# Performance work log

Measured on AMD Instinct MI355X. Metric: run time of the kernel, lower is better.

## Reference

```python
import jax, jax.numpy as jnp
import numpy as np

B, S, D, H = 8, 1024, 1024, 16
DH = D // H  # 64
LN_EPS = 1e-5


def setup_inputs() -> dict:
    key = jax.random.key(0)
    ks = jax.random.split(key, 12)
    w = lambda k, shape: (jax.random.normal(k, shape, dtype=jnp.float32) * 0.02)
    return {
        "key": jax.random.normal(ks[0], (B, S, D), dtype=jnp.float32),
        "value": jax.random.normal(ks[1], (B, S, D), dtype=jnp.float32),
        "query": jax.random.normal(ks[2], (B, S, D), dtype=jnp.float32),
        "atten_mask": jax.random.randint(ks[3], (B, S, S), 0, 2).astype(bool),
        "Wk": w(ks[4], (D, D)), "bk": jnp.zeros((D,), jnp.float32),
        "Wv": w(ks[5], (D, D)), "bv": jnp.zeros((D,), jnp.float32),
        "Wq": w(ks[6], (D, D)), "bq": jnp.zeros((D,), jnp.float32),
        "Wf": w(ks[7], (D, D)), "bf": jnp.zeros((D,), jnp.float32),
        "gamma": jnp.ones((D,), jnp.float32),
        "beta": jnp.zeros((D,), jnp.float32),
    }


def reference(key, value, query, atten_mask, Wk, bk, Wv, bv, Wq, bq, Wf, bf, gamma, beta):
    residual = query
    k = key @ Wk + bk      # [B,S,D]
    v = value @ Wv + bv
    q = query @ Wq + bq
    # Faithful to the original: raw .view(B*H, -1, d) reshape, NO head transpose.
    k = k.reshape(B * H, S, DH)
    v = v.reshape(B * H, S, DH)
    q = q.reshape(B * H, S, DH)
    # torch .repeat(H,1,1) tiles along batch dim -> head bh uses mask[bh % B]
    mask = jnp.tile(atten_mask, (H, 1, 1))  # [B*H, S, S]
    scale = (DH // H) ** (-0.5)  # quirky original scaling: (64//16)**-0.5 = 0.5
    scores = jnp.einsum('bqd,bkd->bqk', q, k) * scale  # [B*H, S, S]
    scores = jnp.where(mask, jnp.float32(-1e6), scores)
    attention = jax.nn.softmax(scores, axis=2)
    context = jnp.einsum('bqk,bkd->bqd', attention, v)  # [B*H, S, DH]
    context = context.reshape(B, S, D)
    out = context @ Wf + bf
    out = residual + out
    # LayerNorm over last dim
    mu = jnp.mean(out, axis=-1, keepdims=True)
    var = jnp.var(out, axis=-1, keepdims=True)
    out = (out - mu) * jax.lax.rsqrt(var + LN_EPS) * gamma + beta
    return out, attention
```

## Files before the change

### kernel.cpp

```cpp
#include <hip/hip_runtime.h>


typedef unsigned short u16;
typedef unsigned long long u64;
typedef __attribute__((ext_vector_type(8))) short bf16x8;
typedef __attribute__((ext_vector_type(4))) float f32x4;

#define MFMA_BF16(a, b, c) __builtin_amdgcn_mfma_f32_16x16x32_bf16((a), (b), (c), 0, 0, 0)

__device__ __forceinline__ u16 f2bf(float f) {
  unsigned u = __float_as_uint(f);
  u += 0x7fffu + ((u >> 16) & 1u);
  return (u16)(u >> 16);
}
__device__ __forceinline__ float bf2f(u16 b) {
  return __uint_as_float(((unsigned)b) << 16);
}
__device__ __forceinline__ unsigned cvt_pk_bf16(float lo, float hi) {
  unsigned r;
  asm("v_cvt_pk_bf16_f32 %0, %1, %2" : "=v"(r) : "v"(lo), "v"(hi));
  return r;
}
__device__ __forceinline__ void gload_lds16(const u16* g, u16* l) {
  __builtin_amdgcn_global_load_lds(
      (const __attribute__((address_space(1))) void*)g,
      (__attribute__((address_space(3))) void*)l, 16, 0, 0);
}

static constexpr size_t MD = 8192ull * 1024ull;
static constexpr size_t DD = 1024ull * 1024ull;
static constexpr float SCL = 0.72134752044f;

__global__ __launch_bounds__(256) void cvt_k(const float* __restrict__ K,
                                             const float* __restrict__ V,
                                             const float* __restrict__ Q,
                                             u16* __restrict__ O) {
  const int z = blockIdx.z;
  const float* src = (z == 0) ? K : ((z == 1) ? V : Q);
  const size_t i = ((size_t)blockIdx.x * 256 + threadIdx.x) * 4;
  const float4 v = *reinterpret_cast<const float4*>(src + i);
  ushort4 o;
  o.x = f2bf(v.x); o.y = f2bf(v.y); o.z = f2bf(v.z); o.w = f2bf(v.w);
  *reinterpret_cast<ushort4*>(O + (size_t)z * MD + i) = o;
}

__global__ __launch_bounds__(256) void wt_k(const float* __restrict__ Wk,
                                            const float* __restrict__ Wv,
                                            const float* __restrict__ Wq,
                                            const float* __restrict__ Wf,
                                            u16* __restrict__ WT) {
  const int z = blockIdx.z;
  const float* W = (z == 0) ? Wk : ((z == 1) ? Wv : ((z == 2) ? Wq : Wf));
  __shared__ float tile[32][33];
  const int k0 = blockIdx.y * 32, n0 = blockIdx.x * 32;
  const int r = threadIdx.x >> 5, c = threadIdx.x & 31;
#pragma unroll
  for (int rr = r; rr < 32; rr += 8)
    tile[rr][c] = W[(size_t)(k0 + rr) * 1024 + n0 + c];
  __syncthreads();
#pragma unroll
  for (int rr = r; rr < 32; rr += 8)
    WT[(size_t)z * DD + (size_t)(n0 + rr) * 1024 + k0 + c] = f2bf(tile[c][rr]);
}

__global__ __launch_bounds__(256) void mb_k(const unsigned char* __restrict__ mask8,
                                            u64* __restrict__ mb) {
  __shared__ int mflag;
  if (threadIdx.x == 0) {
    const unsigned* mw = reinterpret_cast<const unsigned*>(mask8);
    int allW = 1;
    for (int i = 0; i < 64; ++i) {
      const unsigned v = mw[i];
      if (v != 0u && v != 1u && v != 0x3F800000u) allW = 0;
    }
    mflag = allW;
  }
  __syncthreads();
  const int wide = mflag;
  const size_t wi = (size_t)blockIdx.x * 256 + threadIdx.x;
  const size_t src0 = wi * 64;
  u64 bits = 0ull;
  if (!wide) {
    const uint4* p = reinterpret_cast<const uint4*>(mask8 + src0);
#pragma unroll
    for (int q = 0; q < 4; ++q) {
      const uint4 v = p[q];
      const unsigned vv[4] = {v.x, v.y, v.z, v.w};
#pragma unroll
      for (int k = 0; k < 4; ++k) {
        unsigned tt = vv[k];
        tt |= tt >> 4; tt |= tt >> 2; tt |= tt >> 1;
        tt &= 0x01010101u;
        const unsigned nib =
            (tt & 1u) | ((tt >> 7) & 2u) | ((tt >> 14) & 4u) | ((tt >> 21) & 8u);
        bits |= (u64)nib << (q * 16 + k * 4);
      }
    }
  } else {
    const unsigned* p = reinterpret_cast<const unsigned*>(mask8) + src0;
#pragma unroll
    for (int k = 0; k < 64; ++k)
      bits |= (u64)(p[k] != 0u) << k;
  }
  mb[wi] = bits;
}

template <int EPI>
__global__ __launch_bounds__(256) void gemm_bt(
    const u16* __restrict__ A0, const u16* __restrict__ B0,
    const float* __restrict__ bias0, const float* __restrict__ bias1,
    const float* __restrict__ bias2, u16* __restrict__ Obf,
    const float* __restrict__ resid) {
  __shared__ __align__(16) u16 As[128 * 32];
  __shared__ __align__(16) u16 Bs[128 * 32];
  const int z = blockIdx.z;
  const u16* A = A0 + (size_t)z * MD;
  const u16* Bt = B0 + (size_t)z * DD;
  const float* bias = (z == 0) ? bias0 : ((z == 1) ? bias1 : bias2);
  const int t = threadIdx.x;
  const int m0 = blockIdx.y * 128, n0 = blockIdx.x * 128;
  const int w = t >> 6, lane = t & 63, lr = lane & 15, lk = lane >> 4;
  const int wm = (w >> 1) * 64, wn = (w & 1) * 64;
  const int srow = lane >> 2, scol = (lane & 3) * 8;

  f32x4 acc[4][4] = {};

  for (int k0 = 0; k0 < 1024; k0 += 32) {
    __syncthreads();
#pragma unroll
    for (int it = 0; it < 2; ++it) {
      const int c = w * 2 + it;
      gload_lds16(A + (size_t)(m0 + 16 * c + srow) * 1024 + k0 + scol,
                  &As[c * 512 + lane * 8]);
      gload_lds16(Bt + (size_t)(n0 + 16 * c + srow) * 1024 + k0 + scol,
                  &Bs[c * 512 + lane * 8]);
    }
    __syncthreads();
    bf16x8 af[4], bfr[4];
#pragma unroll
    for (int i = 0; i < 4; ++i)
      af[i] = *reinterpret_cast<const bf16x8*>(&As[(wm + i * 16 + lr) * 32 + lk * 8]);
#pragma unroll
    for (int j = 0; j < 4; ++j)
      bfr[j] = *reinterpret_cast<const bf16x8*>(&Bs[(wn + j * 16 + lr) * 32 + lk * 8]);
#pragma unroll
    for (int i = 0; i < 4; ++i) {
#pragma unroll
      for (int j = 0; j < 4; ++j)
        acc[i][j] = MFMA_BF16(af[i], bfr[j], acc[i][j]);
    }
  }

#pragma unroll
  for (int i = 0; i < 4; ++i) {
#pragma unroll
    for (int j = 0; j < 4; ++j) {
#pragma unroll
      for (int r = 0; r < 4; ++r) {
        const int row = m0 + wm + i * 16 + lk * 4 + r;
        const int col = n0 + wn + j * 16 + lr;
        const size_t idx = (size_t)row * 1024 + col;
        const float v = acc[i][j][r] + bias[col];
        if constexpr (EPI == 0) {
          Obf[(size_t)z * MD + idx] = f2bf(v);
        } else {
          Obf[idx] = f2bf(v + resid[idx]);
        }
      }
    }
  }
}

__global__ __launch_bounds__(256) void vt_k(const u16* __restrict__ VP,
                                            u16* __restrict__ VTo) {
  __shared__ __align__(16) u16 tile[64][72];
  const int t = threadIdx.x;
  const int bh = blockIdx.y, p0 = blockIdx.x * 64;
  const int b = bh >> 4, shi = bh & 15;
  const size_t hb = (size_t)b * 1048576 + (size_t)shi * 65536;
#pragma unroll
  for (int it = 0; it < 2; ++it) {
    const int c = t + it * 256;
    const int row = c >> 3, f8 = (c & 7) * 8;
    const int p = p0 + row;
    *reinterpret_cast<int4*>(&tile[row][f8]) = *reinterpret_cast<const int4*>(
        VP + hb + (size_t)(p >> 4) * 1024 + (p & 15) * 64 + f8);
  }
  __syncthreads();
#pragma unroll
  for (int it = 0; it < 2; ++it) {
    const int c = t + it * 256;
    const int f = c >> 3, pc = (c & 7) * 8;
    __align__(16) u16 tmp[8];
#pragma unroll
    for (int i = 0; i < 8; ++i) tmp[i] = tile[pc + i][f];
    *reinterpret_cast<int4*>(VTo + (size_t)bh * 65536 + (size_t)f * 1024 + p0 + pc) =
        *reinterpret_cast<int4*>(tmp);
  }
}

__global__ __launch_bounds__(512, 4) void attn_k(
    const u16* __restrict__ QP, const u16* __restrict__ KP,
    const u16* __restrict__ VT, const u64* __restrict__ mb,
    float* __restrict__ attnOut, u16* __restrict__ ctx) {
  __shared__ __align__(16) u16 Ps[32 * 1024];
  __shared__ float red[8][2][16];

  const int t = threadIdx.x;
  const int qt = blockIdx.x;
  const int bh = blockIdx.y;
  const int q0 = qt * 32;
  const int b = bh >> 4, shi = bh & 15;
  const size_t hb = (size_t)b * 1048576 + (size_t)shi * 65536;
  const u64* mrow = mb + (size_t)(shi & 7) * 16384;

  const int w = t >> 6, lane = t & 63, lr = lane & 15, lk = lane >> 4;
  const int qsw = (lr & 7) << 3;

  bf16x8 qf[2][2];
#pragma unroll
  for (int rg = 0; rg < 2; ++rg) {
    const u16* qb = QP + hb + (size_t)(qt * 2 + rg) * 1024 + lr * 64 + lk * 8;
    qf[rg][0] = *reinterpret_cast<const bf16x8*>(qb);
    qf[rg][1] = *reinterpret_cast<const bf16x8*>(qb + 32);
  }

  float psum[2] = {0.f, 0.f};

#pragma unroll
  for (int ki = 0; ki < 2; ++ki) {
    const int kt = w * 2 + ki;
    const u16* kb = KP + hb + (size_t)(kt * 4) * 1024 + lr * 64 + lk * 8;
    bf16x8 kf[4][2];
#pragma unroll
    for (int j = 0; j < 4; ++j) {
      kf[j][0] = *reinterpret_cast<const bf16x8*>(kb + j * 1024);
      kf[j][1] = *reinterpret_cast<const bf16x8*>(kb + j * 1024 + 32);
    }
#pragma unroll
    for (int rg = 0; rg < 2; ++rg) {
      f32x4 sf[4];
#pragma unroll
      for (int j = 0; j < 4; ++j) {
        f32x4 a = {};
        a = MFMA_BF16(kf[j][0], qf[rg][0], a);
        a = MFMA_BF16(kf[j][1], qf[rg][1], a);
        sf[j] = a;
      }
      const u64 mw = mrow[(size_t)(q0 + rg * 16 + lr) * 16 + kt];
#pragma unroll
      for (int j = 0; j < 4; ++j) {
        float p[4];
#pragma unroll
        for (int r = 0; r < 4; ++r) {
          const unsigned bit = (unsigned)(mw >> (j * 16 + lk * 4 + r)) & 1u;
          const float sel = bit ? -__builtin_inff() : 0.0f;
          p[r] = __builtin_amdgcn_exp2f(fmaf(sf[j][r], SCL, sel));
          psum[rg] += p[r];
        }
        const unsigned lo = cvt_pk_bf16(p[0], p[1]);
        const unsigned hi = cvt_pk_bf16(p[2], p[3]);
        const int kel = (kt * 64 + j * 16 + lk * 4) ^ qsw;
        *reinterpret_cast<u64*>(&Ps[(rg * 16 + lr) * 1024 + kel]) =
            (u64)lo | ((u64)hi << 32);
      }
    }
  }
#pragma unroll
  for (int rg = 0; rg < 2; ++rg) {
    psum[rg] += __shfl_xor(psum[rg], 16, 64);
    psum[rg] += __shfl_xor(psum[rg], 32, 64);
  }
  if (lane < 16) { red[w][0][lr] = psum[0]; red[w][1][lr] = psum[1]; }
  __syncthreads();

  float rsl = 0.f;
  if (lane < 32) {
#pragma unroll
    for (int w2 = 0; w2 < 8; ++w2) rsl += red[w2][lane >> 4][lane & 15];
  }
  const float rinvl = (rsl > 0.f) ? __builtin_amdgcn_rcpf(rsl) : 0.f;

  if (w < 4) {
    const int cg = w * 16;
    const u16* vb = VT + (size_t)bh * 65536 + (size_t)(cg + lr) * 1024 + lk * 8;
    f32x4 cacc[2][2] = {};
#pragma unroll
    for (int kk = 0; kk < 32; ++kk) {
      const int kel = (kk * 32 + lk * 8) ^ qsw;
      const bf16x8 vf = *reinterpret_cast<const bf16x8*>(vb + kk * 32);
      const bf16x8 pf0 = *reinterpret_cast<const bf16x8*>(&Ps[lr * 1024 + kel]);
      const bf16x8 pf1 = *reinterpret_cast<const bf16x8*>(&Ps[(16 + lr) * 1024 + kel]);
      cacc[0][kk & 1] = MFMA_BF16(pf0, vf, cacc[0][kk & 1]);
      cacc[1][kk & 1] = MFMA_BF16(pf1, vf, cacc[1][kk & 1]);
    }
#pragma unroll
    for (int rg = 0; rg < 2; ++rg) {
#pragma unroll
      for (int r = 0; r < 4; ++r) {
        const int lrow = rg * 16 + lk * 4 + r;
        const float ri = __shfl(rinvl, lrow, 64);
        const float cv = cacc[rg][0][r] + cacc[rg][1][r];
        const int p = q0 + lrow;
        ctx[hb + (size_t)(p >> 4) * 1024 + (size_t)(p & 15) * 64 + cg + lr] =
            f2bf(cv * ri);
      }
    }
  } else {
    const int t2 = t - 256;
    float* aout = attnOut + (size_t)bh * 1048576 + (size_t)q0 * 1024;
#pragma unroll
    for (int i = 0; i < 32; ++i) {
      const int asw = (i & 7) << 3;
      const float ri = __shfl(rinvl, i, 64);
      const u64 p4 = *reinterpret_cast<const u64*>(&Ps[i * 1024 + ((t2 * 4) ^ asw)]);
      f32x4 o;
      o[0] = bf2f((u16)(p4 & 0xffffu)) * ri;
      o[1] = bf2f((u16)((p4 >> 16) & 0xffffu)) * ri;
      o[2] = bf2f((u16)((p4 >> 32) & 0xffffu)) * ri;
      o[3] = bf2f((u16)(p4 >> 48)) * ri;
      __builtin_nontemporal_store(
          o, reinterpret_cast<f32x4*>(aout + (size_t)i * 1024 + t2 * 4));
    }
  }
}

__global__ __launch_bounds__(256) void ln_k(const u16* __restrict__ X,
                                            const float* __restrict__ gamma,
                                            const float* __restrict__ beta,
                                            float* __restrict__ Y) {
  const int row = blockIdx.x, t = threadIdx.x;
  const size_t base = (size_t)row * 1024;
  const u64 xw = *reinterpret_cast<const u64*>(X + base + t * 4);
  float x0 = bf2f((u16)(xw & 0xffffu));
  float x1 = bf2f((u16)((xw >> 16) & 0xffffu));
  float x2 = bf2f((u16)((xw >> 32) & 0xffffu));
  float x3 = bf2f((u16)(xw >> 48));
  float s = x0 + x1 + x2 + x3;
  float s2 = x0 * x0 + x1 * x1 + x2 * x2 + x3 * x3;
#pragma unroll
  for (int d = 1; d < 64; d <<= 1) {
    s += __shfl_xor(s, d, 64);
    s2 += __shfl_xor(s2, d, 64);
  }
  __shared__ float red[8];
  const int w = t >> 6;
  if ((t & 63) == 0) { red[w] = s; red[4 + w] = s2; }
  __syncthreads();
  s = red[0] + red[1] + red[2] + red[3];
  s2 = red[4] + red[5] + red[6] + red[7];
  const float mu = s * (1.f / 1024.f);
  const float var = s2 * (1.f / 1024.f) - mu * mu;
  const float inv = rsqrtf(var + 1e-5f);
  const float4 g = *reinterpret_cast<const float4*>(gamma + t * 4);
  const float4 be = *reinterpret_cast<const float4*>(beta + t * 4);
  float4 y;
  y.x = (x0 - mu) * inv * g.x + be.x;
  y.y = (x1 - mu) * inv * g.y + be.y;
  y.z = (x2 - mu) * inv * g.z + be.z;
  y.w = (x3 - mu) * inv * g.w + be.w;
  *reinterpret_cast<float4*>(Y + base + t * 4) = y;
}

extern "C" void kernel_launch(void* const* d_in, const int* in_sizes, int n_in,
                              void* d_out, int out_size, void* d_ws, size_t ws_size,
                              hipStream_t stream) {
  const float* keyF = (const float*)d_in[0];
  const float* valueF = (const float*)d_in[1];
  const float* queryF = (const float*)d_in[2];
  const unsigned char* mask8 = (const unsigned char*)d_in[3];
  const float* Wk = (const float*)d_in[4];
  const float* bk = (const float*)d_in[5];
  const float* Wv = (const float*)d_in[6];
  const float* bv = (const float*)d_in[7];
  const float* Wq = (const float*)d_in[8];
  const float* bq = (const float*)d_in[9];
  const float* Wf = (const float*)d_in[10];
  const float* bfp = (const float*)d_in[11];
  const float* gamma = (const float*)d_in[12];
  const float* beta = (const float*)d_in[13];

  char* ws = (char*)d_ws;
  u16* Xbf = (u16*)(ws);
  u16* WT = (u16*)(ws + 50331648);
  u16* KP = (u16*)(ws + 58720256);
  u16* VP = (u16*)(ws + 75497472);
  u16* QP = (u16*)(ws + 92274688);
  u16* VT = (u16*)(ws + 109051904);
  u64* MB = (u64*)(ws + 125829120);
  u16* CTX = (u16*)(ws);
  u16* PRELN = (u16*)(ws + 16777216);

  float* outF = (float*)d_out;
  float* attnF = outF + 8388608;

  cvt_k<<<dim3(8192, 1, 3), 256, 0, stream>>>(keyF, valueF, queryF, Xbf);
  wt_k<<<dim3(32, 32, 4), 256, 0, stream>>>(Wk, Wv, Wq, Wf, WT);
  mb_k<<<dim3(512), 256, 0, stream>>>(mask8, MB);
  gemm_bt<0><<<dim3(8, 64, 3), 256, 0, stream>>>(Xbf, WT, bk, bv, bq, KP, nullptr);
  vt_k<<<dim3(16, 128), 256, 0, stream>>>(VP, VT);
  attn_k<<<dim3(32, 128), 512, 0, stream>>>(QP, KP, VT, MB, attnF, CTX);
  gemm_bt<1><<<dim3(8, 64, 1), 256, 0, stream>>>(CTX, WT + 3 * DD, bfp, bfp, bfp,
                                                 PRELN, queryF);
  ln_k<<<dim3(8192), 256, 0, stream>>>(PRELN, gamma, beta, outF);
}
```

Baseline: 338.1 us.

## Fuse fp32-to-bf16 input conversion into projection GEMM, merge weight/mask prep kernels

Drops the separate kernel that converted key/value/query to bf16. The projection GEMM now loads fp32 activations straight into registers, converts them with packed bf16 instructions, and writes them into a padded LDS tile. The weight-transpose and mask-bitpack kernels are merged into one launch. This saves a full fp32 read plus bf16 write and read of three 8M-element tensors and two kernel launches. In exchange the A-operand load is now synchronous register traffic at twice the byte width, repeated for each of the 8 column tiles, rather than async global-to-LDS loads.

```diff
diff --git a/kernel.cpp b/kernel.cpp
--- a/kernel.cpp
+++ b/kernel.cpp
@@ -31,42 +31,29 @@
 static constexpr size_t DD = 1024ull * 1024ull;
 static constexpr float SCL = 0.72134752044f;
 
-__global__ __launch_bounds__(256) void cvt_k(const float* __restrict__ K,
-                                             const float* __restrict__ V,
-                                             const float* __restrict__ Q,
-                                             u16* __restrict__ O) {
+__global__ __launch_bounds__(256) void wtmb_k(
+    const float* __restrict__ Wk, const float* __restrict__ Wv,
+    const float* __restrict__ Wq, const float* __restrict__ Wf,
+    const unsigned char* __restrict__ mask8, u16* __restrict__ WT,
+    u64* __restrict__ mb) {
+  __shared__ float tile[32][33];
+  __shared__ int mflag;
   const int z = blockIdx.z;
-  const float* src = (z == 0) ? K : ((z == 1) ? V : Q);
-  const size_t i = ((size_t)blockIdx.x * 256 + threadIdx.x) * 4;
-  const float4 v = *reinterpret_cast<const float4*>(src + i);
-  ushort4 o;
-  o.x = f2bf(v.x); o.y = f2bf(v.y); o.z = f2bf(v.z); o.w = f2bf(v.w);
-  *reinterpret_cast<ushort4*>(O + (size_t)z * MD + i) = o;
-}
-
-__global__ __launch_bounds__(256) void wt_k(const float* __restrict__ Wk,
-                                            const float* __restrict__ Wv,
-                                            const float* __restrict__ Wq,
-                                            const float* __restrict__ Wf,
-                                            u16* __restrict__ WT) {
-  const int z = blockIdx.z;
-  const float* W = (z == 0) ? Wk : ((z == 1) ? Wv : ((z == 2) ? Wq : Wf));
-  __shared__ float tile[32][33];
-  const int k0 = blockIdx.y * 32, n0 = blockIdx.x * 32;
-  const int r = threadIdx.x >> 5, c = threadIdx.x & 31;
-#pragma unroll
-  for (int rr = r; rr < 32; rr += 8)
-    tile[rr][c] = W[(size_t)(k0 + rr) * 1024 + n0 + c];
-  __syncthreads();
-#pragma unroll
-  for (int rr = r; rr < 32; rr += 8)
-    WT[(size_t)z * DD + (size_t)(n0 + rr) * 1024 + k0 + c] = f2bf(tile[c][rr]);
-}
-
-__global__ __launch_bounds__(256) void mb_k(const unsigned char* __restrict__ mask8,
-                                            u64* __restrict__ mb) {
-  __shared__ int mflag;
-  if (threadIdx.x == 0) {
+  const int t = threadIdx.x;
+  if (z < 4) {
+    const float* W = (z == 0) ? Wk : ((z == 1) ? Wv : ((z == 2) ? Wq : Wf));
+    const int k0 = blockIdx.y * 32, n0 = blockIdx.x * 32;
+    const int r = t >> 5, c = t & 31;
+#pragma unroll
+    for (int rr = r; rr < 32; rr += 8)
+      tile[rr][c] = W[(size_t)(k0 + rr) * 1024 + n0 + c];
+    __syncthreads();
+#pragma unroll
+    for (int rr = r; rr < 32; rr += 8)
+      WT[(size_t)z * DD + (size_t)(n0 + rr) * 1024 + k0 + c] = f2bf(tile[c][rr]);
+    return;
+  }
+  if (t == 0) {
     const unsigned* mw = reinterpret_cast<const unsigned*>(mask8);
     int allW = 1;
     for (int i = 0; i < 64; ++i) {
@@ -76,8 +63,9 @@
     mflag = allW;
   }
   __syncthreads();
+  if (t >= 128) return;
   const int wide = mflag;
-  const size_t wi = (size_t)blockIdx.x * 256 + threadIdx.x;
+  const size_t wi = (size_t)(blockIdx.y * 32 + blockIdx.x) * 128 + t;
   const size_t src0 = wi * 64;
   u64 bits = 0ull;
   if (!wide) {
@@ -105,16 +93,15 @@
   mb[wi] = bits;
 }
 
-template <int EPI>
-__global__ __launch_bounds__(256) void gemm_bt(
-    const u16* __restrict__ A0, const u16* __restrict__ B0,
+__global__ __launch_bounds__(256) void gemm_proj(
+    const float* __restrict__ K0, const float* __restrict__ V0,
+    const float* __restrict__ Q0, const u16* __restrict__ B0,
     const float* __restrict__ bias0, const float* __restrict__ bias1,
-    const float* __restrict__ bias2, u16* __restrict__ Obf,
-    const float* __restrict__ resid) {
-  __shared__ __align__(16) u16 As[128 * 32];
+    const float* __restrict__ bias2, u16* __restrict__ Obf) {
+  __shared__ __align__(16) u16 As[128 * 40];
   __shared__ __align__(16) u16 Bs[128 * 32];
   const int z = blockIdx.z;
-  const u16* A = A0 + (size_t)z * MD;
+  const float* Af = (z == 0) ? K0 : ((z == 1) ? V0 : Q0);
   const u16* Bt = B0 + (size_t)z * DD;
   const float* bias = (z == 0) ? bias0 : ((z == 1) ? bias1 : bias2);
   const int t = threadIdx.x;
@@ -122,6 +109,72 @@
   const int w = t >> 6, lane = t & 63, lr = lane & 15, lk = lane >> 4;
   const int wm = (w >> 1) * 64, wn = (w & 1) * 64;
   const int srow = lane >> 2, scol = (lane & 3) * 8;
+  const int arow = t >> 3, acol = (t & 7) * 4;
+
+  f32x4 acc[4][4] = {};
+
+  for (int k0 = 0; k0 < 1024; k0 += 32) {
+    float4 av[4];
+#pragma unroll
+    for (int p = 0; p < 4; ++p)
+      av[p] = *reinterpret_cast<const float4*>(
+          Af + (size_t)(m0 + p * 32 + arow) * 1024 + k0 + acol);
+    __syncthreads();
+#pragma unroll
+    for (int it = 0; it < 2; ++it) {
+      const int c = w * 2 + it;
+      gload_lds16(Bt + (size_t)(n0 + 16 * c + srow) * 1024 + k0 + scol,
+                  &Bs[c * 512 + lane * 8]);
+    }
+#pragma unroll
+    for (int p = 0; p < 4; ++p) {
+      const unsigned lo = cvt_pk_bf16(av[p].x, av[p].y);
+      const unsigned hi = cvt_pk_bf16(av[p].z, av[p].w);
+      *reinterpret_cast<u64*>(&As[(p * 32 + arow) * 40 + acol]) =
+          (u64)lo | ((u64)hi << 32);
+    }
+    __syncthreads();
+    bf16x8 af[4], bfr[4];
+#pragma unroll
+    for (int i = 0; i < 4; ++i)
+      af[i] = *reinterpret_cast<const bf16x8*>(&As[(wm + i * 16 + lr) * 40 + lk * 8]);
+#pragma unroll
+    for (int j = 0; j < 4; ++j)
+      bfr[j] = *reinterpret_cast<const bf16x8*>(&Bs[(wn + j * 16 + lr) * 32 + lk * 8]);
+#pragma unroll
+    for (int i = 0; i < 4; ++i) {
+#pragma unroll
+      for (int j = 0; j < 4; ++j)
+        acc[i][j] = MFMA_BF16(af[i], bfr[j], acc[i][j]);
+    }
+  }
+
+#pragma unroll
+  for (int i = 0; i < 4; ++i) {
+#pragma unroll
+    for (int j = 0; j < 4; ++j) {
+#pragma unroll
+      for (int r = 0; r < 4; ++r) {
+        const int row = m0 + wm + i * 16 + lk * 4 + r;
+        const int col = n0 + wn + j * 16 + lr;
+        Obf[(size_t)z * MD + (size_t)row * 1024 + col] =
+            f2bf(acc[i][j][r] + bias[col]);
+      }
+    }
+  }
+}
+
+__global__ __launch_bounds__(256) void gemm_fin(
+    const u16* __restrict__ A, const u16* __restrict__ Bt,
+    const float* __restrict__ bias, u16* __restrict__ Obf,
+    const float* __restrict__ resid) {
+  __shared__ __align__(16) u16 As[128 * 32];
+  __shared__ __align__(16) u16 Bs[128 * 32];
+  const int t = threadIdx.x;
+  const int m0 = blockIdx.y * 128, n0 = blockIdx.x * 128;
+  const int w = t >> 6, lane = t & 63, lr = lane & 15, lk = lane >> 4;
+  const int wm = (w >> 1) * 64, wn = (w & 1) * 64;
+  const int srow = lane >> 2, scol = (lane & 3) * 8;
 
   f32x4 acc[4][4] = {};
 
@@ -160,12 +213,7 @@
         const int row = m0 + wm + i * 16 + lk * 4 + r;
         const int col = n0 + wn + j * 16 + lr;
         const size_t idx = (size_t)row * 1024 + col;
-        const float v = acc[i][j][r] + bias[col];
-        if constexpr (EPI == 0) {
-          Obf[(size_t)z * MD + idx] = f2bf(v);
-        } else {
-          Obf[idx] = f2bf(v + resid[idx]);
-        }
+        Obf[idx] = f2bf(acc[i][j][r] + bias[col] + resid[idx]);
       }
     }
   }
@@ -381,7 +429,6 @@
   const float* beta = (const float*)d_in[13];
 
   char* ws = (char*)d_ws;
-  u16* Xbf = (u16*)(ws);
   u16* WT = (u16*)(ws + 50331648);
   u16* KP = (u16*)(ws + 58720256);
   u16* VP = (u16*)(ws + 75497472);
@@ -394,13 +441,11 @@
   float* outF = (float*)d_out;
   float* attnF = outF + 8388608;
 
-  cvt_k<<<dim3(8192, 1, 3), 256, 0, stream>>>(keyF, valueF, queryF, Xbf);
-  wt_k<<<dim3(32, 32, 4), 256, 0, stream>>>(Wk, Wv, Wq, Wf, WT);
-  mb_k<<<dim3(512), 256, 0, stream>>>(mask8, MB);
-  gemm_bt<0><<<dim3(8, 64, 3), 256, 0, stream>>>(Xbf, WT, bk, bv, bq, KP, nullptr);
+  wtmb_k<<<dim3(32, 32, 5), 256, 0, stream>>>(Wk, Wv, Wq, Wf, mask8, WT, MB);
+  gemm_proj<<<dim3(8, 64, 3), 256, 0, stream>>>(keyF, valueF, queryF, WT,
+                                                bk, bv, bq, KP);
   vt_k<<<dim3(16, 128), 256, 0, stream>>>(VP, VT);
   attn_k<<<dim3(32, 128), 512, 0, stream>>>(QP, KP, VT, MB, attnF, CTX);
-  gemm_bt<1><<<dim3(8, 64, 1), 256, 0, stream>>>(CTX, WT + 3 * DD, bfp, bfp, bfp,
-                                                 PRELN, queryF);
+  gemm_fin<<<dim3(8, 64), 256, 0, stream>>>(CTX, WT + 3 * DD, bfp, PRELN, queryF);
   ln_k<<<dim3(8192), 256, 0, stream>>>(PRELN, gamma, beta, outF);
 }
```

New measurement: 361.4 us. 6.9% more time.
